# Kernel optimization log

Hardware: AMD Instinct MI355X
Metric: run time of the kernel (lower is better)

## Reference

```python
import jax, jax.numpy as jnp
import numpy as np

N_NODES = 100000
N_EDGES = 1600000
NFEAT, NHID, NOUT = 128, 64, 32


def setup_inputs() -> dict:
    key = jax.random.key(0)
    ks = jax.random.split(key, 8)
    x = jax.random.normal(ks[0], (N_NODES, NFEAT), dtype=jnp.float32)
    adj_vals = jax.random.uniform(ks[1], (N_EDGES,), dtype=jnp.float32)
    W1 = jax.random.normal(ks[2], (NFEAT, NHID), dtype=jnp.float32) * (1.0 / np.sqrt(NFEAT))
    b1 = jnp.zeros((NHID,), dtype=jnp.float32)
    W2 = jax.random.normal(ks[3], (NHID, NOUT), dtype=jnp.float32) * (1.0 / np.sqrt(NHID))
    b2 = jnp.zeros((NOUT,), dtype=jnp.float32)
    edge_src = jax.random.randint(ks[4], (N_EDGES,), 0, N_NODES, dtype=jnp.int32)
    edge_dst = jax.random.randint(ks[5], (N_EDGES,), 0, N_NODES, dtype=jnp.int32)
    return {"x": x, "adj_vals": adj_vals, "W1": W1, "b1": b1, "W2": W2,
            "b2": b2, "edge_src": edge_src, "edge_dst": edge_dst}


def spmm(vals, src, dst, dense, n_nodes):
    # out[i, :] = sum_{e : dst[e]==i} vals[e] * dense[src[e], :]
    gathered = dense[src] * vals[:, None]          # [E, D] gather (memory-bound)
    return jax.ops.segment_sum(gathered, dst, num_segments=n_nodes)


def reference(x, adj_vals, W1, b1, W2, b2, edge_src, edge_dst):
    # GraphConvolution 1: support = x @ W1; out = adj @ support + b1; relu
    h = spmm(adj_vals, edge_src, edge_dst, x @ W1, N_NODES) + b1
    h = jax.nn.relu(h)
    # dropout is identity in eval mode (training=False)
    # GraphConvolution 2
    out = spmm(adj_vals, edge_src, edge_dst, h @ W2, N_NODES) + b2
    return out
```

## Files before the change

kernel.cpp:

```cpp
#include <hip/hip_runtime.h>
#include <hip/hip_fp16.h>

#define N_NODES 100000
#define N_EDGES 1600000
#define NFEAT 128
#define NHID 64
#define NOUT 32

#define NPB 256
#define NB ((N_NODES + NPB - 1) / NPB)
#define CAP 4608
#define CCH 4096
#define NCH ((N_EDGES + CCH - 1) / CCH)
#define G1B ((N_NODES / 16 + 7) / 8)

typedef _Float16 half8 __attribute__((ext_vector_type(8)));
typedef float floatx4 __attribute__((ext_vector_type(4)));

__device__ __forceinline__ int wave_incl_scan(int v, int lane) {
#pragma unroll
    for (int d = 1; d < 64; d <<= 1) {
        int t = __shfl_up(v, d, 64);
        if (lane >= d) v += t;
    }
    return v;
}
__device__ __forceinline__ int block_excl_scan_512(int tsum, int tid, int* w8) {
    const int lane = tid & 63, wid = tid >> 6;
    int incl = wave_incl_scan(tsum, lane);
    if (lane == 63) w8[wid] = incl;
    __syncthreads();
    int wbase = 0;
#pragma unroll
    for (int i = 0; i < 7; ++i)
        if (wid > i) wbase += w8[i];
    return wbase + incl - tsum;
}

__global__ __launch_bounds__(64) void prep_kernel(const float* __restrict__ W1,
                                                  const float* __restrict__ W2,
                                                  __half* __restrict__ wfrag,
                                                  __half* __restrict__ w2frag,
                                                  int* __restrict__ gcur) {
    const int l = threadIdx.x;
    const int b = blockIdx.x;
    if (b < 16) {
        const int ks = b >> 2, ct = b & 3;
        const int kb = ks * 32 + (l >> 4) * 8;
        const int c  = ct * 16 + (l & 15);
        union { __half2 h2[4]; uint4 u; } pk;
#pragma unroll
        for (int j = 0; j < 4; ++j)
            pk.h2[j] = __floats2half2_rn(W1[(kb + 2 * j) * NHID + c],
                                         W1[(kb + 2 * j + 1) * NHID + c]);
        *(uint4*)&wfrag[((size_t)b * 64 + l) * 8] = pk.u;
    } else if (b < 20) {
        const int bb = b - 16;
        const int ks = bb >> 1, ct = bb & 1;
        const int kb = ks * 32 + (l >> 4) * 8;
        const int c  = ct * 16 + (l & 15);
        union { __half2 h2[4]; uint4 u; } pk;
#pragma unroll
        for (int j = 0; j < 4; ++j)
            pk.h2[j] = __floats2half2_rn(W2[(kb + 2 * j) * NOUT + c],
                                         W2[(kb + 2 * j + 1) * NOUT + c]);
        *(uint4*)&w2frag[((size_t)bb * 64 + l) * 8] = pk.u;
    } else {
        int i = (b - 20) * 64 + l;
        if (i < NB) gcur[i] = i * CAP;
    }
}

__global__ __launch_bounds__(512) void g1cs_kernel(const float* __restrict__ x,
                                                   const __half* __restrict__ wfrag,
                                                   __half* __restrict__ support,
                                                   const float* __restrict__ vals,
                                                   const int* __restrict__ src,
                                                   const int* __restrict__ dst,
                                                   int* __restrict__ gcur,
                                                   uint2* __restrict__ recsC) {
    __shared__ int cnt[NB];
    __shared__ int pos[NB];
    const int tid = threadIdx.x;

    if (blockIdx.x < NCH) {
        const int cbase0 = blockIdx.x * CCH;
        for (int i = tid; i < NB; i += 512) cnt[i] = 0;
        int dstv[CCH / 512];
        __syncthreads();
#pragma unroll
        for (int k = 0; k < CCH / 512; ++k) {
            int e = cbase0 + k * 512 + tid;
            int d = (e < N_EDGES) ? dst[e] : -1;
            dstv[k] = d;
            if (d >= 0) atomicAdd(&cnt[d >> 8], 1);
        }
        __syncthreads();
        for (int b = tid; b < NB; b += 512) {
            int c = cnt[b];
            pos[b] = c ? atomicAdd(&gcur[b], c) : 0;
        }
        __syncthreads();
#pragma unroll
        for (int k = 0; k < CCH / 512; ++k) {
            int e = cbase0 + k * 512 + tid;
            int d = dstv[k];
            if (d >= 0) {
                int b = d >> 8;
                int slot = atomicAdd(&pos[b], 1);
                if (slot < (b + 1) * CAP)
                    recsC[slot] = make_uint2((unsigned)src[e] |
                                             ((unsigned)(d & (NPB - 1)) << 17),
                                             __float_as_uint(vals[e]));
            }
        }
    } else {
        const int lane = tid & 63;
        const int tile = (blockIdx.x - NCH) * 8 + (tid >> 6);
        const int n0 = tile * 16;
        if (n0 >= N_NODES) return;

        half8 a[4][4];
#pragma unroll
        for (int ks = 0; ks < 4; ++ks)
#pragma unroll
            for (int ct = 0; ct < 4; ++ct)
                a[ks][ct] = *(const half8*)&wfrag[((size_t)(ks * 4 + ct) * 64 + lane) * 8];

        floatx4 acc[4];
#pragma unroll
        for (int ct = 0; ct < 4; ++ct) acc[ct] = (floatx4){0.f, 0.f, 0.f, 0.f};

        const int node = n0 + (lane & 15);
        const float* xrow = x + (size_t)node * NFEAT + (lane >> 4) * 8;

#pragma unroll
        for (int ks = 0; ks < 4; ++ks) {
            float4 f0 = *(const float4*)(xrow + ks * 32);
            float4 f1 = *(const float4*)(xrow + ks * 32 + 4);
            union { __half2 h2[4]; half8 v; } bv;
            bv.h2[0] = __floats2half2_rn(f0.x, f0.y);
            bv.h2[1] = __floats2half2_rn(f0.z, f0.w);
            bv.h2[2] = __floats2half2_rn(f1.x, f1.y);
            bv.h2[3] = __floats2half2_rn(f1.z, f1.w);
#pragma unroll
            for (int ct = 0; ct < 4; ++ct)
                acc[ct] = __builtin_amdgcn_mfma_f32_16x16x32_f16(a[ks][ct], bv.v, acc[ct], 0, 0, 0);
        }

        __half* srow = support + (size_t)node * NHID + (lane >> 4) * 4;
#pragma unroll
        for (int ct = 0; ct < 4; ++ct) {
            union { __half2 h2[2]; uint2 u; } pk;
            pk.h2[0] = __floats2half2_rn(acc[ct][0], acc[ct][1]);
            pk.h2[1] = __floats2half2_rn(acc[ct][2], acc[ct][3]);
            *(uint2*)&srow[ct * 16] = pk.u;
        }
    }
}

__global__ __launch_bounds__(512) void fine_sort_kernel(const int* __restrict__ gcur,
                                                        const uint2* __restrict__ recsC,
                                                        unsigned* __restrict__ recs2,
                                                        int* __restrict__ offs,
                                                        int* __restrict__ ends) {
    __shared__ int cnt[NPB];
    __shared__ int cur[NPB];
    __shared__ int w8[8];
    const int tid = threadIdx.x;
    const int b = blockIdx.x;
    const int s = b * CAP;
    const int e = min(gcur[b], s + CAP);
    if (tid < NPB) cnt[tid] = 0;
    __syncthreads();
    for (int i = s + tid; i < e; i += 512)
        atomicAdd(&cnt[(recsC[i].x >> 17) & (NPB - 1)], 1);
    __syncthreads();
    int v = (tid < NPB) ? cnt[tid] : 0;
    int excl = block_excl_scan_512(v, tid, w8);
    if (tid < NPB) {
        cur[tid] = excl;
        const int node = b * NPB + tid;
        if (node < N_NODES) {
            offs[node] = s + excl;
            ends[node] = s + excl + v;
        }
    }
    __syncthreads();
    for (int i = s + tid; i < e; i += 512) {
        uint2 r = recsC[i];
        int dl = (r.x >> 17) & (NPB - 1);
        unsigned hb = (unsigned)__half_as_ushort(__float2half(__uint_as_float(r.y))) & 0x7FFFu;
        int p = atomicAdd(&cur[dl], 1);
        recs2[s + p] = (r.x & 0x1FFFFu) | (hb << 17);
    }
}

__global__ __launch_bounds__(256) void spmm1_kernel(const int* __restrict__ offs,
                                                    const int* __restrict__ ends,
                                                    const unsigned* __restrict__ recs,
                                                    const __half* __restrict__ dense,
                                                    const float* __restrict__ b1,
                                                    __half* __restrict__ h) {
    __shared__ float red[4][8][65];
    const int tid = threadIdx.x;
    const int lane = tid & 63;
    const int wid = tid >> 6;
    const int d = blockIdx.x * 4 + wid;
    if (d >= N_NODES) return;
    const int g = lane >> 3, q = lane & 7;
    __half2 hacc[4];
#pragma unroll
    for (int j = 0; j < 4; ++j) hacc[j] = __half2half2(__float2half(0.f));

    const int start = offs[d], end = ends[d];
    for (int e = start + g; e < end; e += 8) {
        unsigned r = recs[e];
        __half2 hv2 = __half2half2(__ushort_as_half((unsigned short)(r >> 17)));
        union { uint4 u; __half2 h2[4]; } rw;
        rw.u = *(const uint4*)((const char*)dense + ((size_t)(r & 0x1FFFFu) << 7) + (q << 4));
#pragma unroll
        for (int j = 0; j < 4; ++j)
            hacc[j] = __hfma2(rw.h2[j], hv2, hacc[j]);
    }
#pragma unroll
    for (int j = 0; j < 4; ++j) {
        float2 f = __half22float2(hacc[j]);
        red[wid][g][q * 8 + 2 * j]     = f.x;
        red[wid][g][q * 8 + 2 * j + 1] = f.y;
    }
    __builtin_amdgcn_wave_barrier();
    float s = 0.f;
#pragma unroll
    for (int gg = 0; gg < 8; ++gg) s += red[wid][gg][lane];
    float hv = fmaxf(s + b1[lane], 0.f);
    h[(size_t)d * NHID + lane] = __float2half(hv);
}

__global__ __launch_bounds__(256) void gemm2_kernel(const __half* __restrict__ h,
                                                    const __half* __restrict__ w2frag,
                                                    __half* __restrict__ s2) {
    const int lane = threadIdx.x & 63;
    const int tile = blockIdx.x * 4 + (threadIdx.x >> 6);
    const int n0 = tile * 16;
    if (n0 >= N_NODES) return;

    half8 a[2][2];
#pragma unroll
    for (int ks = 0; ks < 2; ++ks)
#pragma unroll
        for (int ct = 0; ct < 2; ++ct)
            a[ks][ct] = *(const half8*)&w2frag[((size_t)(ks * 2 + ct) * 64 + lane) * 8];

    floatx4 acc[2];
#pragma unroll
    for (int ct = 0; ct < 2; ++ct) acc[ct] = (floatx4){0.f, 0.f, 0.f, 0.f};

    const int node = n0 + (lane & 15);
    const __half* hrow = h + (size_t)node * NHID + (lane >> 4) * 8;

#pragma unroll
    for (int ks = 0; ks < 2; ++ks) {
        half8 bv = *(const half8*)(hrow + ks * 32);
#pragma unroll
        for (int ct = 0; ct < 2; ++ct)
            acc[ct] = __builtin_amdgcn_mfma_f32_16x16x32_f16(a[ks][ct], bv, acc[ct], 0, 0, 0);
    }

    __half* srow = s2 + (size_t)node * NOUT + (lane >> 4) * 4;
#pragma unroll
    for (int ct = 0; ct < 2; ++ct) {
        union { __half2 h2[2]; uint2 u; } pk;
        pk.h2[0] = __floats2half2_rn(acc[ct][0], acc[ct][1]);
        pk.h2[1] = __floats2half2_rn(acc[ct][2], acc[ct][3]);
        *(uint2*)&srow[ct * 16] = pk.u;
    }
}

__global__ __launch_bounds__(256) void spmm2_kernel(const int* __restrict__ offs,
                                                    const int* __restrict__ ends,
                                                    const unsigned* __restrict__ recs,
                                                    const __half* __restrict__ dense,
                                                    const float* __restrict__ b2,
                                                    float* __restrict__ out) {
    __shared__ float red[4][16][33];
    const int tid = threadIdx.x;
    const int lane = tid & 63;
    const int wid = tid >> 6;
    const int d = blockIdx.x * 4 + wid;
    if (d >= N_NODES) return;
    const int g = lane >> 2, q4 = lane & 3;
    __half2 hacc[4];
#pragma unroll
    for (int j = 0; j < 4; ++j) hacc[j] = __half2half2(__float2half(0.f));

    const int start = offs[d], end = ends[d];
    const char* dbase = (const char*)dense + (q4 << 4);
    for (int e = start + g; e < end; e += 16) {
        unsigned r = recs[e];
        __half2 hv2 = __half2half2(__ushort_as_half((unsigned short)(r >> 17)));
        union { uint4 u; __half2 h2[4]; } rw;
        rw.u = *(const uint4*)(dbase + ((size_t)(r & 0x1FFFFu) << 6));
#pragma unroll
        for (int j = 0; j < 4; ++j)
            hacc[j] = __hfma2(rw.h2[j], hv2, hacc[j]);
    }
#pragma unroll
    for (int j = 0; j < 4; ++j) {
        float2 f = __half22float2(hacc[j]);
        red[wid][g][q4 * 8 + 2 * j]     = f.x;
        red[wid][g][q4 * 8 + 2 * j + 1] = f.y;
    }
    __builtin_amdgcn_wave_barrier();
    const int c = lane & 31, chunk = lane >> 5;
    float s = 0.f;
#pragma unroll
    for (int t = 0; t < 8; ++t) s += red[wid][chunk * 8 + t][c];
    s += __shfl_xor(s, 32, 64);
    if (chunk == 0) out[(size_t)d * NOUT + c] = s + b2[c];
}

extern "C" void kernel_launch(void* const* d_in, const int* in_sizes, int n_in,
                              void* d_out, int out_size, void* d_ws, size_t ws_size,
                              hipStream_t stream) {
    const float* x        = (const float*)d_in[0];
    const float* adj_vals = (const float*)d_in[1];
    const float* W1       = (const float*)d_in[2];
    const float* b1       = (const float*)d_in[3];
    const float* W2       = (const float*)d_in[4];
    const float* b2       = (const float*)d_in[5];
    const int*   esrc     = (const int*)d_in[6];
    const int*   edst     = (const int*)d_in[7];
    float*       out      = (float*)d_out;

    char* W = (char*)d_ws;
    __half*   support = (__half*)W;
    __half*   h       = (__half*)(W + 12800000);
    uint2*    recsC   = (uint2*)(W + 25600000);
    unsigned* recs2   = (unsigned*)(W + 25600000 + (size_t)NB * CAP * 8);
    int*      IW      = (int*)(W + 25600000 + (size_t)NB * CAP * 12);
    int*      offs    = IW;
    int*      ends    = IW + 100032;
    int*      gcur    = IW + 200064;
    __half*   wfrag   = (__half*)(IW + 200064 + 512);
    __half*   w2frag  = wfrag + 8192;
    __half*   s2      = support;

    prep_kernel<<<20 + (NB + 63) / 64, 64, 0, stream>>>(W1, W2, wfrag, w2frag, gcur);

    g1cs_kernel<<<NCH + G1B, 512, 0, stream>>>(x, wfrag, support,
                                               adj_vals, esrc, edst, gcur, recsC);

    fine_sort_kernel<<<NB, 512, 0, stream>>>(gcur, recsC, recs2, offs, ends);

    spmm1_kernel<<<(N_NODES + 3) / 4, 256, 0, stream>>>(offs, ends, recs2,
                                                        support, b1, h);

    gemm2_kernel<<<(N_NODES / 16 + 3) / 4, 256, 0, stream>>>(h, w2frag, s2);

    spmm2_kernel<<<(N_NODES + 3) / 4, 256, 0, stream>>>(offs, ends, recs2,
                                                        s2, b2, out);
}
```

Before: 131.6 us.

## Split coarse bucket sort into two radix passes with fewer buckets

Replaces the single 391-bucket scatter pass with a two-level partition: edges are first scattered into 25 super-buckets of 4096 nodes, and a new pass then splits each super-bucket into 16 buckets of 256 nodes before the fine sort. This shrinks the per-block shared counters and global atomics and should make scatter writes more contiguous per block. In exchange it adds a kernel launch and an extra read/write pass over all 1.6M edge records, plus a larger workspace.

New measurement: 132.8 us. No clear change (+0.9%).

```diff
diff --git a/kernel.cpp b/kernel.cpp
--- a/kernel.cpp
+++ b/kernel.cpp
@@ -10,8 +10,11 @@
 #define NPB 256
 #define NB ((N_NODES + NPB - 1) / NPB)
 #define CAP 4608
+#define NSB 25
+#define SCAPA 69632
 #define CCH 4096
 #define NCH ((N_EDGES + CCH - 1) / CCH)
+#define SBCH 17
 #define G1B ((N_NODES / 16 + 7) / 8)
 
 typedef _Float16 half8 __attribute__((ext_vector_type(8)));
@@ -41,7 +44,8 @@
                                                   const float* __restrict__ W2,
                                                   __half* __restrict__ wfrag,
                                                   __half* __restrict__ w2frag,
-                                                  int* __restrict__ gcur) {
+                                                  int* __restrict__ gcurA,
+                                                  int* __restrict__ gcurB) {
     const int l = threadIdx.x;
     const int b = blockIdx.x;
     if (b < 16) {
@@ -67,7 +71,8 @@
         *(uint4*)&w2frag[((size_t)bb * 64 + l) * 8] = pk.u;
     } else {
         int i = (b - 20) * 64 + l;
-        if (i < NB) gcur[i] = i * CAP;
+        if (i < NB) gcurB[i] = i * CAP;
+        else if (i < NB + NSB) gcurA[i - NB] = (i - NB) * SCAPA;
     }
 }
 
@@ -77,15 +82,15 @@
                                                    const float* __restrict__ vals,
                                                    const int* __restrict__ src,
                                                    const int* __restrict__ dst,
-                                                   int* __restrict__ gcur,
-                                                   uint2* __restrict__ recsC) {
-    __shared__ int cnt[NB];
-    __shared__ int pos[NB];
+                                                   int* __restrict__ gcurA,
+                                                   uint2* __restrict__ recsA) {
+    __shared__ int cnt[32];
+    __shared__ int pos[32];
     const int tid = threadIdx.x;
 
     if (blockIdx.x < NCH) {
         const int cbase0 = blockIdx.x * CCH;
-        for (int i = tid; i < NB; i += 512) cnt[i] = 0;
+        if (tid < 32) cnt[tid] = 0;
         int dstv[CCH / 512];
         __syncthreads();
 #pragma unroll
@@ -93,12 +98,12 @@
             int e = cbase0 + k * 512 + tid;
             int d = (e < N_EDGES) ? dst[e] : -1;
             dstv[k] = d;
-            if (d >= 0) atomicAdd(&cnt[d >> 8], 1);
+            if (d >= 0) atomicAdd(&cnt[d >> 12], 1);
         }
         __syncthreads();
-        for (int b = tid; b < NB; b += 512) {
-            int c = cnt[b];
-            pos[b] = c ? atomicAdd(&gcur[b], c) : 0;
+        if (tid < NSB) {
+            int c = cnt[tid];
+            pos[tid] = c ? atomicAdd(&gcurA[tid], c) : 0;
         }
         __syncthreads();
 #pragma unroll
@@ -106,11 +111,11 @@
             int e = cbase0 + k * 512 + tid;
             int d = dstv[k];
             if (d >= 0) {
-                int b = d >> 8;
-                int slot = atomicAdd(&pos[b], 1);
-                if (slot < (b + 1) * CAP)
-                    recsC[slot] = make_uint2((unsigned)src[e] |
-                                             ((unsigned)(d & (NPB - 1)) << 17),
+                int sb = d >> 12;
+                int slot = atomicAdd(&pos[sb], 1);
+                if (slot < (sb + 1) * SCAPA)
+                    recsA[slot] = make_uint2((unsigned)src[e] |
+                                             ((unsigned)(d & 4095) << 17),
                                              __float_as_uint(vals[e]));
             }
         }
@@ -155,6 +160,52 @@
             pk.h2[0] = __floats2half2_rn(acc[ct][0], acc[ct][1]);
             pk.h2[1] = __floats2half2_rn(acc[ct][2], acc[ct][3]);
             *(uint2*)&srow[ct * 16] = pk.u;
+        }
+    }
+}
+
+__global__ __launch_bounds__(512) void passB_kernel(const int* __restrict__ gcurA,
+                                                    const uint2* __restrict__ recsA,
+                                                    int* __restrict__ gcurB,
+                                                    uint2* __restrict__ recsB) {
+    __shared__ int cnt[16];
+    __shared__ int pos[16];
+    const int tid = threadIdx.x;
+    const int sb = blockIdx.x / SBCH;
+    const int ch = blockIdx.x - sb * SBCH;
+    const int base = sb * SCAPA + ch * 4096;
+    const int fill = gcurA[sb];
+    const int end = min(base + 4096, fill);
+
+    if (tid < 16) cnt[tid] = 0;
+    uint2 rr[4096 / 512];
+    __syncthreads();
+#pragma unroll
+    for (int k = 0; k < 4096 / 512; ++k) {
+        int i = base + k * 512 + tid;
+        if (i < end) {
+            uint2 r = recsA[i];
+            rr[k] = r;
+            atomicAdd(&cnt[(r.x >> 25) & 15], 1);
+        }
+    }
+    __syncthreads();
+    if (tid < 16) {
+        int c = cnt[tid];
+        pos[tid] = c ? atomicAdd(&gcurB[sb * 16 + tid], c) : 0;
+    }
+    __syncthreads();
+#pragma unroll
+    for (int k = 0; k < 4096 / 512; ++k) {
+        int i = base + k * 512 + tid;
+        if (i < end) {
+            uint2 r = rr[k];
+            int b16 = (r.x >> 25) & 15;
+            int gb = sb * 16 + b16;
+            int slot = atomicAdd(&pos[b16], 1);
+            if (slot < (gb + 1) * CAP)
+                recsB[slot] = make_uint2((r.x & 0x1FFFFu) |
+                                         (((r.x >> 17) & 255u) << 17), r.y);
         }
     }
 }
@@ -336,22 +387,29 @@
     char* W = (char*)d_ws;
     __half*   support = (__half*)W;
     __half*   h       = (__half*)(W + 12800000);
-    uint2*    recsC   = (uint2*)(W + 25600000);
-    unsigned* recs2   = (unsigned*)(W + 25600000 + (size_t)NB * CAP * 8);
-    int*      IW      = (int*)(W + 25600000 + (size_t)NB * CAP * 12);
+    uint2*    recsA   = (uint2*)(W + 25600000);
+    uint2*    recsB   = (uint2*)(W + 25600000 + (size_t)NSB * SCAPA * 8);
+    unsigned* recs2   = (unsigned*)(W + 25600000 + (size_t)NSB * SCAPA * 8
+                                    + (size_t)NB * CAP * 8);
+    int*      IW      = (int*)(W + 25600000 + (size_t)NSB * SCAPA * 8
+                               + (size_t)NB * CAP * 12);
     int*      offs    = IW;
     int*      ends    = IW + 100032;
-    int*      gcur    = IW + 200064;
-    __half*   wfrag   = (__half*)(IW + 200064 + 512);
+    int*      gcurA   = IW + 200064;
+    int*      gcurB   = gcurA + 64;
+    __half*   wfrag   = (__half*)(gcurB + 512);
     __half*   w2frag  = wfrag + 8192;
     __half*   s2      = support;
 
-    prep_kernel<<<20 + (NB + 63) / 64, 64, 0, stream>>>(W1, W2, wfrag, w2frag, gcur);
+    prep_kernel<<<20 + (NB + NSB + 63) / 64, 64, 0, stream>>>(W1, W2, wfrag, w2frag,
+                                                              gcurA, gcurB);
 
     g1cs_kernel<<<NCH + G1B, 512, 0, stream>>>(x, wfrag, support,
-                                               adj_vals, esrc, edst, gcur, recsC);
-
-    fine_sort_kernel<<<NB, 512, 0, stream>>>(gcur, recsC, recs2, offs, ends);
+                                               adj_vals, esrc, edst, gcurA, recsA);
+
+    passB_kernel<<<NSB * SBCH, 512, 0, stream>>>(gcurA, recsA, gcurB, recsB);
+
+    fine_sort_kernel<<<NB, 512, 0, stream>>>(gcurB, recsB, recs2, offs, ends);
 
     spmm1_kernel<<<(N_NODES + 3) / 4, 256, 0, stream>>>(offs, ends, recs2,
                                                         support, b1, h);
```
